# Kernel tuning notes

Measured on AMD Instinct MI355X. Metric: run time of the kernel, lower is better.

Reference implementation:

```python
import jax, jax.numpy as jnp
import numpy as np

N_NODES = 100000
N_EDGES = 3200000
D_IN = 256
D_OUT = 256


def setup_inputs() -> dict:
    key = jax.random.key(0)
    k1, k2, k3, k4, k5, k6 = jax.random.split(key, 6)
    x = jax.random.normal(k1, (N_NODES, D_IN), dtype=jnp.float32)
    adj_row = jnp.sort(jax.random.randint(k2, (N_EDGES,), 0, N_NODES, dtype=jnp.int64))
    adj_col = jax.random.randint(k3, (N_EDGES,), 0, N_NODES, dtype=jnp.int64)
    adj_val = jax.random.uniform(k4, (N_EDGES,), dtype=jnp.float32)
    stdv = 1.0 / np.sqrt(D_OUT)
    weight = jax.random.uniform(k5, (D_IN, D_OUT), dtype=jnp.float32, minval=-stdv, maxval=stdv)
    bias = jax.random.uniform(k6, (D_OUT,), dtype=jnp.float32, minval=-stdv, maxval=stdv)
    return {"x": x, "adj_row": adj_row, "adj_col": adj_col, "adj_val": adj_val,
            "weight": weight, "bias": bias}


def reference(x, adj_row, adj_col, adj_val, weight, bias):
    # support = x @ W   -> [N, D_OUT]
    support = x @ weight
    # output = spmm(adj, support): gather source rows, scale by edge value,
    # segment-reduce into destination rows.
    msgs = adj_val[:, None] * support[adj_col]          # [E, D_OUT]
    output = jax.ops.segment_sum(msgs, adj_row, num_segments=N_NODES)
    return output + bias
```

## Files before the change

kernel.cpp:

```cpp
#include <hip/hip_runtime.h>
#include <hip/hip_bf16.h>

#define D_FEAT 256

typedef __attribute__((ext_vector_type(8))) __bf16 bf16x8;
typedef __attribute__((ext_vector_type(4))) __bf16 bf16x4;
typedef __attribute__((ext_vector_type(4))) float f32x4;

__global__ __launch_bounds__(256) void prep(
    const int* __restrict__ rows, int E, int* __restrict__ ptr, int N,
    const float* __restrict__ W, __bf16* __restrict__ Wt, int RB) {
  const int b = blockIdx.x;
  if (b < RB) {
    const int n = b * 256 + threadIdx.x;
    if (n > N) return;
    int lo = 0, hi = E;
    while (lo < hi) {
      const int mid = (lo + hi) >> 1;
      if (rows[mid] < n) lo = mid + 1; else hi = mid;
    }
    ptr[n] = lo;
  } else {
    const int n = b - RB;
    const int k = threadIdx.x;
    Wt[n * 256 + k] = (__bf16)W[k * 256 + n];
  }
}

#define APITCH 40

__global__ __launch_bounds__(256) void gemm_mfma(
    const float* __restrict__ X, const __bf16* __restrict__ Wt,
    __bf16* __restrict__ S, int M) {
  __shared__ __bf16 As[128 * APITCH];
  __shared__ __bf16 Bs[128 * APITCH];
  const int tid = threadIdx.x;
  const int wave = tid >> 6;
  const int lane = tid & 63;
  const int m0 = blockIdx.y * 128;
  const int n0 = blockIdx.x * 128;

  f32x4 acc[2][8] = {};

  const int l15 = lane & 15;
  const int kh8 = (lane >> 4) * 8;

  const int r = tid >> 1;
  const int kh = (tid & 1) * 16;
  const int gr = m0 + r;
  const bool valid = gr < M;
  const float* xsrc = X + (size_t)(valid ? gr : 0) * D_FEAT + kh;

  float4 pre[4];
#pragma unroll
  for (int q = 0; q < 4; ++q)
    pre[q] = valid ? *reinterpret_cast<const float4*>(xsrc + q * 4)
                   : make_float4(0.f, 0.f, 0.f, 0.f);

  const int nr = tid >> 1;
  const int qb = (tid & 1) * 16;

  for (int k0 = 0; k0 < D_FEAT; k0 += 32) {
    const __bf16* wsrc = Wt + (size_t)(n0 + nr) * D_FEAT + k0 + qb;
    bf16x8 wb0 = *reinterpret_cast<const bf16x8*>(wsrc);
    bf16x8 wb1 = *reinterpret_cast<const bf16x8*>(wsrc + 8);

    bf16x8 a0, a1;
    a0[0] = (__bf16)pre[0].x; a0[1] = (__bf16)pre[0].y;
    a0[2] = (__bf16)pre[0].z; a0[3] = (__bf16)pre[0].w;
    a0[4] = (__bf16)pre[1].x; a0[5] = (__bf16)pre[1].y;
    a0[6] = (__bf16)pre[1].z; a0[7] = (__bf16)pre[1].w;
    a1[0] = (__bf16)pre[2].x; a1[1] = (__bf16)pre[2].y;
    a1[2] = (__bf16)pre[2].z; a1[3] = (__bf16)pre[2].w;
    a1[4] = (__bf16)pre[3].x; a1[5] = (__bf16)pre[3].y;
    a1[6] = (__bf16)pre[3].z; a1[7] = (__bf16)pre[3].w;
    *reinterpret_cast<bf16x8*>(&As[r * APITCH + kh]) = a0;
    *reinterpret_cast<bf16x8*>(&As[r * APITCH + kh + 8]) = a1;
    *reinterpret_cast<bf16x8*>(&Bs[nr * APITCH + qb]) = wb0;
    *reinterpret_cast<bf16x8*>(&Bs[nr * APITCH + qb + 8]) = wb1;

    const bool have = (k0 + 32) < D_FEAT;
    float4 nxt[4];
    if (have && valid) {
#pragma unroll
      for (int q = 0; q < 4; ++q)
        nxt[q] = *reinterpret_cast<const float4*>(xsrc + k0 + 32 + q * 4);
    }
    __syncthreads();

    bf16x8 a[2], b[8];
#pragma unroll
    for (int rg = 0; rg < 2; ++rg)
      a[rg] = *reinterpret_cast<const bf16x8*>(
          &As[(wave * 32 + rg * 16 + l15) * APITCH + kh8]);
#pragma unroll
    for (int cg = 0; cg < 8; ++cg)
      b[cg] = *reinterpret_cast<const bf16x8*>(
          &Bs[(cg * 16 + l15) * APITCH + kh8]);
#pragma unroll
    for (int rg = 0; rg < 2; ++rg)
#pragma unroll
      for (int cg = 0; cg < 8; ++cg)
        acc[rg][cg] = __builtin_amdgcn_mfma_f32_16x16x32_bf16(
            b[cg], a[rg], acc[rg][cg], 0, 0, 0);
    __syncthreads();

    if (have && valid) {
#pragma unroll
      for (int q = 0; q < 4; ++q) pre[q] = nxt[q];
    }
  }

#pragma unroll
  for (int rg = 0; rg < 2; ++rg) {
    const int m = m0 + wave * 32 + rg * 16 + l15;
    if (m < M) {
#pragma unroll
      for (int cg = 0; cg < 8; ++cg) {
        const int nb = n0 + cg * 16 + (lane >> 4) * 4;
        bf16x4 p;
#pragma unroll
        for (int rr = 0; rr < 4; ++rr) p[rr] = (__bf16)acc[rg][cg][rr];
        *reinterpret_cast<bf16x4*>(&S[(size_t)m * D_FEAT + nb]) = p;
      }
    }
  }
}

__global__ __launch_bounds__(256) void spmm_rows(
    const __bf16* __restrict__ S, const int* __restrict__ ptr,
    const int* __restrict__ col, const float* __restrict__ val,
    const float* __restrict__ bias, float* __restrict__ out, int N) {
  const int wave = threadIdx.x >> 6;
  const int lane = threadIdx.x & 63;
  const int n = blockIdx.x * 4 + wave;
  if (n >= N) return;

  const int e0 = ptr[n];
  const int e1 = ptr[n + 1];
  const int hw = lane >> 5;
  const int f0 = (lane & 31) * 8;

  float acc[8] = {};
  const int deg = e1 - e0;
  const int elast = e1 - 1;
  const int nit = (deg + 15) >> 4;

  int e = e0;
  for (int b = 0; b < nit; ++b, e += 16) {
    int cc[8];
    float vv[8];
#pragma unroll
    for (int i = 0; i < 8; ++i) {
      int ee = e + 2 * i + hw;
      const bool ok = ee <= elast;
      ee = ok ? ee : elast;
      cc[i] = col[ee];
      vv[i] = ok ? val[ee] : 0.f;
    }
#pragma unroll
    for (int i = 0; i < 8; ++i) {
      bf16x8 s = *reinterpret_cast<const bf16x8*>(S + (size_t)cc[i] * D_FEAT + f0);
#pragma unroll
      for (int j = 0; j < 8; ++j) acc[j] += vv[i] * (float)s[j];
    }
  }

#pragma unroll
  for (int j = 0; j < 8; ++j) acc[j] += __shfl(acc[j], lane ^ 32, 64);

  const int fw = f0 + hw * 4;
  const float4 b = *reinterpret_cast<const float4*>(bias + fw);
  const float r0 = hw ? acc[4] : acc[0];
  const float r1 = hw ? acc[5] : acc[1];
  const float r2 = hw ? acc[6] : acc[2];
  const float r3 = hw ? acc[7] : acc[3];
  f32x4 o;
  o[0] = r0 + b.x; o[1] = r1 + b.y; o[2] = r2 + b.z; o[3] = r3 + b.w;
  __builtin_nontemporal_store(
      o, reinterpret_cast<f32x4*>(out + (size_t)n * D_FEAT + fw));
}

extern "C" void kernel_launch(void* const* d_in, const int* in_sizes, int n_in,
                              void* d_out, int out_size, void* d_ws, size_t ws_size,
                              hipStream_t stream) {
  const float* x       = (const float*)d_in[0];
  const int*   adj_row = (const int*)d_in[1];
  const int*   adj_col = (const int*)d_in[2];
  const float* adj_val = (const float*)d_in[3];
  const float* weight  = (const float*)d_in[4];
  const float* bias    = (const float*)d_in[5];
  float*       out     = (float*)d_out;

  const int N = in_sizes[0] / D_FEAT;
  const int E = in_sizes[1];

  __bf16* Wt      = (__bf16*)d_ws;
  __bf16* support = Wt + 256 * 256;
  int*    rowptr  = (int*)(support + (size_t)N * D_FEAT);

  const int RB = (N + 1 + 255) / 256;
  prep<<<RB + 256, 256, 0, stream>>>(adj_row, E, rowptr, N, weight, Wt, RB);

  {
    dim3 grid(D_FEAT / 128, (N + 127) / 128);
    gemm_mfma<<<grid, 256, 0, stream>>>(x, Wt, support, N);
  }
  {
    const int blocks = (N + 3) / 4;
    spmm_rows<<<blocks, 256, 0, stream>>>(support, rowptr, adj_col, adj_val,
                                          bias, out, N);
  }
}
```

Before: 278.4 us.

## Widen GEMM tile to full 256 output columns so X is read once

The GEMM block now computes all 256 output columns for its 128 rows instead of splitting N into two 128-wide tiles across blocks. Each fp32 X row is loaded and converted to bf16 only once rather than twice, which cuts the dominant global read traffic of the GEMM. In exchange, accumulator registers double (32 f32x4 per thread), the LDS B tile doubles, and the grid is half as many blocks. This may lower occupancy or cause register spilling.

```diff
diff --git a/kernel.cpp b/kernel.cpp
--- a/kernel.cpp
+++ b/kernel.cpp
@@ -33,14 +33,13 @@
     const float* __restrict__ X, const __bf16* __restrict__ Wt,
     __bf16* __restrict__ S, int M) {
   __shared__ __bf16 As[128 * APITCH];
-  __shared__ __bf16 Bs[128 * APITCH];
+  __shared__ __bf16 Bs[256 * APITCH];
   const int tid = threadIdx.x;
   const int wave = tid >> 6;
   const int lane = tid & 63;
   const int m0 = blockIdx.y * 128;
-  const int n0 = blockIdx.x * 128;
-
-  f32x4 acc[2][8] = {};
+
+  f32x4 acc[2][16] = {};
 
   const int l15 = lane & 15;
   const int kh8 = (lane >> 4) * 8;
@@ -57,13 +56,14 @@
     pre[q] = valid ? *reinterpret_cast<const float4*>(xsrc + q * 4)
                    : make_float4(0.f, 0.f, 0.f, 0.f);
 
-  const int nr = tid >> 1;
-  const int qb = (tid & 1) * 16;
+  const int nr = tid;
 
   for (int k0 = 0; k0 < D_FEAT; k0 += 32) {
-    const __bf16* wsrc = Wt + (size_t)(n0 + nr) * D_FEAT + k0 + qb;
+    const __bf16* wsrc = Wt + (size_t)nr * D_FEAT + k0;
     bf16x8 wb0 = *reinterpret_cast<const bf16x8*>(wsrc);
     bf16x8 wb1 = *reinterpret_cast<const bf16x8*>(wsrc + 8);
+    bf16x8 wb2 = *reinterpret_cast<const bf16x8*>(wsrc + 16);
+    bf16x8 wb3 = *reinterpret_cast<const bf16x8*>(wsrc + 24);
 
     bf16x8 a0, a1;
     a0[0] = (__bf16)pre[0].x; a0[1] = (__bf16)pre[0].y;
@@ -76,8 +76,10 @@
     a1[6] = (__bf16)pre[3].z; a1[7] = (__bf16)pre[3].w;
     *reinterpret_cast<bf16x8*>(&As[r * APITCH + kh]) = a0;
     *reinterpret_cast<bf16x8*>(&As[r * APITCH + kh + 8]) = a1;
-    *reinterpret_cast<bf16x8*>(&Bs[nr * APITCH + qb]) = wb0;
-    *reinterpret_cast<bf16x8*>(&Bs[nr * APITCH + qb + 8]) = wb1;
+    *reinterpret_cast<bf16x8*>(&Bs[nr * APITCH]) = wb0;
+    *reinterpret_cast<bf16x8*>(&Bs[nr * APITCH + 8]) = wb1;
+    *reinterpret_cast<bf16x8*>(&Bs[nr * APITCH + 16]) = wb2;
+    *reinterpret_cast<bf16x8*>(&Bs[nr * APITCH + 24]) = wb3;
 
     const bool have = (k0 + 32) < D_FEAT;
     float4 nxt[4];
@@ -88,21 +90,20 @@
     }
     __syncthreads();
 
-    bf16x8 a[2], b[8];
+    bf16x8 a[2];
 #pragma unroll
     for (int rg = 0; rg < 2; ++rg)
       a[rg] = *reinterpret_cast<const bf16x8*>(
           &As[(wave * 32 + rg * 16 + l15) * APITCH + kh8]);
 #pragma unroll
-    for (int cg = 0; cg < 8; ++cg)
-      b[cg] = *reinterpret_cast<const bf16x8*>(
+    for (int cg = 0; cg < 16; ++cg) {
+      bf16x8 b = *reinterpret_cast<const bf16x8*>(
           &Bs[(cg * 16 + l15) * APITCH + kh8]);
-#pragma unroll
-    for (int rg = 0; rg < 2; ++rg)
-#pragma unroll
-      for (int cg = 0; cg < 8; ++cg)
-        acc[rg][cg] = __builtin_amdgcn_mfma_f32_16x16x32_bf16(
-            b[cg], a[rg], acc[rg][cg], 0, 0, 0);
+      acc[0][cg] = __builtin_amdgcn_mfma_f32_16x16x32_bf16(
+          b, a[0], acc[0][cg], 0, 0, 0);
+      acc[1][cg] = __builtin_amdgcn_mfma_f32_16x16x32_bf16(
+          b, a[1], acc[1][cg], 0, 0, 0);
+    }
     __syncthreads();
 
     if (have && valid) {
@@ -116,8 +117,8 @@
     const int m = m0 + wave * 32 + rg * 16 + l15;
     if (m < M) {
 #pragma unroll
-      for (int cg = 0; cg < 8; ++cg) {
-        const int nb = n0 + cg * 16 + (lane >> 4) * 4;
+      for (int cg = 0; cg < 16; ++cg) {
+        const int nb = cg * 16 + (lane >> 4) * 4;
         bf16x4 p;
 #pragma unroll
         for (int rr = 0; rr < 4; ++rr) p[rr] = (__bf16)acc[rg][cg][rr];
@@ -203,7 +204,7 @@
   prep<<<RB + 256, 256, 0, stream>>>(adj_row, E, rowptr, N, weight, Wt, RB);
 
   {
-    dim3 grid(D_FEAT / 128, (N + 127) / 128);
+    dim3 grid(1, (N + 127) / 128);
     gemm_mfma<<<grid, 256, 0, stream>>>(x, Wt, support, N);
   }
   {
```

Result: slower. 287.9 us (+3.4%).
